# Kernel optimization log

Measured on AMD Instinct MI355X. Metric: run time of the kernel, lower is better.

The kernel has to match this reference:

```python
import jax, jax.numpy as jnp
import numpy as np

DIM = 128        # per-head dim == model width in this module
Q_HEADS = 16
KV_HEADS = 4
WINDOW = 512
BATCH = 4
SEQ = 2048


def setup_inputs() -> dict:
    key = jax.random.key(0)
    k1, k2, k3 = jax.random.split(key, 3)
    x = jax.random.normal(k1, (BATCH, SEQ, DIM), dtype=jnp.float32)
    # fused qkv weight, stored (in, out) so forward is x @ W_qkv
    W_qkv = jax.random.normal(k2, (DIM, (Q_HEADS + 2 * KV_HEADS) * DIM), dtype=jnp.float32) * (DIM ** -0.5)
    W_proj = jax.random.normal(k3, (Q_HEADS * DIM, DIM), dtype=jnp.float32) * ((Q_HEADS * DIM) ** -0.5)
    return {"x": x, "W_qkv": W_qkv, "W_proj": W_proj}


def _gqa_forward(x, W_qkv, W_proj):
    b, s, d = x.shape
    qkv = x @ W_qkv                                    # [b, s, (Hq+2Hkv)*d]
    qkv = qkv.reshape(b, s, Q_HEADS + 2 * KV_HEADS, d).transpose(0, 2, 1, 3)
    q = qkv[:, :Q_HEADS]                               # [b, Hq, s, d]
    k = qkv[:, Q_HEADS:Q_HEADS + KV_HEADS]             # [b, Hkv, s, d]
    v = qkv[:, Q_HEADS + KV_HEADS:]                    # [b, Hkv, s, d]

    # GQA: repeat kv heads to match q heads
    group = Q_HEADS // KV_HEADS
    k = jnp.repeat(k, group, axis=1)                   # [b, Hq, s, d]
    v = jnp.repeat(v, group, axis=1)

    scale = 1.0 / jnp.sqrt(jnp.float32(d))
    scores = jnp.einsum('bhqd,bhkd->bhqk', q, k) * scale   # [b, Hq, s, s]

    q_idx = jnp.arange(s)[:, None]
    kv_idx = jnp.arange(s)[None, :]
    rel = (q_idx - kv_idx).astype(jnp.float32)         # [s, s]
    # per-head ALiBi slope: exp2(-(h+1)*8/Hq), added (sign matches source)
    h = jnp.arange(Q_HEADS, dtype=jnp.float32)
    slopes = jnp.exp2(-((h + 1.0) * 8.0 / Q_HEADS))    # [Hq]
    scores = scores + slopes[None, :, None, None] * rel[None, None, :, :]

    mask = (q_idx >= kv_idx) & ((q_idx - kv_idx) <= WINDOW)
    scores = jnp.where(mask[None, None], scores, -jnp.inf)
    probs = jax.nn.softmax(scores, axis=-1)

    att = jnp.einsum('bhqk,bhkd->bhqd', probs, v)      # [b, Hq, s, d]
    att = att.transpose(0, 2, 1, 3).reshape(b, s, Q_HEADS * d)
    return att @ W_proj                                # [b, s, d]


def reference(x, W_qkv, W_proj):
    return _gqa_forward(x, W_qkv, W_proj)
```

## Files before the change

### kernel.cpp

```cpp
#include <hip/hip_runtime.h>
#include <math.h>

#define DIM_    128
#define QH_     16
#define KVH_    4
#define WIN_    512
#define BATCH_  4
#define SEQ_    2048
#define QKV_LD  3072
#define ATT_LD  2048

#define NX   (BATCH_*SEQ_*DIM_)
#define NWQ  (DIM_*QKV_LD)
#define NWP  (ATT_LD*DIM_)

typedef __attribute__((ext_vector_type(8))) short short8;
typedef __attribute__((ext_vector_type(4))) float f32x4;
typedef unsigned short u16;
typedef unsigned int u32;

__device__ __forceinline__ u16 f2bf(float f) {
    u32 u = __float_as_uint(f);
    u += 0x7fff + ((u >> 16) & 1);
    return (u16)(u >> 16);
}
__device__ __forceinline__ float bf2f(u16 u) {
    return __uint_as_float(((u32)u) << 16);
}
__device__ __forceinline__ u32 pkbf(float a, float b) {
    u32 r;
    __asm__("v_cvt_pk_bf16_f32 %0, %1, %2" : "=v"(r) : "v"(a), "v"(b));
    return r;
}
#define MFMA16 __builtin_amdgcn_mfma_f32_16x16x32_bf16

#if __has_builtin(__builtin_amdgcn_exp2f)
#define EXP2F __builtin_amdgcn_exp2f
#else
#define EXP2F exp2f
#endif

__device__ __forceinline__ void gload_lds16(const u16* g, u16* l) {
    __builtin_amdgcn_global_load_lds(
        (const __attribute__((address_space(1))) unsigned int*)(const void*)g,
        (__attribute__((address_space(3))) unsigned int*)(void*)l, 16, 0, 0);
}

__global__ __launch_bounds__(256) void prep(
    const float* __restrict__ x, const float* __restrict__ Wqkv,
    const float* __restrict__ Wproj,
    u16* __restrict__ xh, u16* __restrict__ wth, u16* __restrict__ wpth)
{
    if (blockIdx.x < 1024) {
        const size_t t = (size_t)blockIdx.x * 256 + threadIdx.x;
        float4 v = *(const float4*)(x + 4 * t);
        ushort4 o;
        o.x = f2bf(v.x); o.y = f2bf(v.y); o.z = f2bf(v.z); o.w = f2bf(v.w);
        *(ushort4*)(xh + 4 * t) = o;
        return;
    }
    __shared__ float T[32][33];
    int tile = blockIdx.x - 1024;
    const float* src; u16* dst; int K, N;
    if (tile < 384) { src = Wqkv;  dst = wth;  K = 128;  N = 3072; }
    else { tile -= 384; src = Wproj; dst = wpth; K = 2048; N = 128; }
    const int ntile = N >> 5;
    const int k0 = (tile / ntile) << 5, n0 = (tile % ntile) << 5;
    const int tx = threadIdx.x & 31, ty = threadIdx.x >> 5;
    #pragma unroll
    for (int i = 0; i < 4; ++i)
        T[ty + 8 * i][tx] = src[(size_t)(k0 + ty + 8 * i) * N + n0 + tx];
    __syncthreads();
    #pragma unroll
    for (int i = 0; i < 4; ++i)
        dst[(size_t)(n0 + ty + 8 * i) * K + k0 + tx] = f2bf(T[tx][ty + 8 * i]);
}

__global__ __launch_bounds__(256) void gemm1_mfma(
    const u16* __restrict__ xh, const u16* __restrict__ wth,
    u16* __restrict__ qkvb, u16* __restrict__ vg)
{
    const int bn = blockIdx.x * 64;
    const int mc = blockIdx.y * 512;
    const int wv = threadIdx.x >> 6, lane = threadIdx.x & 63;
    const int lo = lane & 15, hi = lane >> 4;
    const int lr = lo, quad = hi;

    short8 bf[4][4];
    #pragma unroll
    for (int nt = 0; nt < 4; ++nt)
        #pragma unroll
        for (int s = 0; s < 4; ++s)
            bf[nt][s] = *(const short8*)(
                wth + (size_t)(bn + nt * 16 + lo) * DIM_ + s * 32 + hi * 8);

    const bool qk = (bn < 2560);
    const u16* aA = xh + (size_t)(mc + wv * 16 + lo) * DIM_ + hi * 8;

#define G1BODY(AF, IT) do {                                                   \
    f32x4 acc[4] = {};                                                        \
    if (qk) {                                                                 \
        _Pragma("unroll")                                                     \
        for (int s = 0; s < 4; ++s)                                           \
            _Pragma("unroll")                                                 \
            for (int nt = 0; nt < 4; ++nt)                                    \
                acc[nt] = MFMA16(bf[nt][s], AF[s], acc[nt], 0, 0, 0);         \
        const int row = mc + (IT) * 64 + wv * 16 + lr;                        \
        u16* dst = qkvb + (size_t)row * QKV_LD + bn + quad * 4;               \
        _Pragma("unroll")                                                     \
        for (int nt = 0; nt < 4; ++nt) {                                      \
            uint2 o;                                                          \
            o.x = pkbf(acc[nt][0], acc[nt][1]);                               \
            o.y = pkbf(acc[nt][2], acc[nt][3]);                               \
            *(uint2*)(dst + nt * 16) = o;                                     \
        }                                                                     \
    } else {                                                                  \
        _Pragma("unroll")                                                     \
        for (int s = 0; s < 4; ++s)                                           \
            _Pragma("unroll")                                                 \
            for (int nt = 0; nt < 4; ++nt)                                    \
                acc[nt] = MFMA16(AF[s], bf[nt][s], acc[nt], 0, 0, 0);         \
        const int m0 = mc + (IT) * 64 + wv * 16 + quad * 4;                   \
        const int bb = m0 >> 11, mseq = m0 & 2047;                            \
        _Pragma("unroll")                                                     \
        for (int nt = 0; nt < 4; ++nt) {                                      \
            const int ncol = bn + nt * 16 + lr - 2560;                        \
            const int kvh = ncol >> 7, d = ncol & 127;                        \
            uint2 o;                                                          \
            o.x = pkbf(acc[nt][0], acc[nt][1]);                               \
            o.y = pkbf(acc[nt][2], acc[nt][3]);                               \
            *(uint2*)(vg + ((size_t)(bb * KVH_ + kvh) * DIM_ + d) * SEQ_      \
                      + mseq) = o;                                            \
        }                                                                     \
    }                                                                         \
} while (0)

    short8 afA[4], afB[4];
    #pragma unroll
    for (int s = 0; s < 4; ++s) afA[s] = *(const short8*)(aA + s * 32);

    #pragma unroll 1
    for (int it = 0; it < 8; it += 2) {
        const u16* aN = aA + (size_t)(it + 1) * 64 * DIM_;
        #pragma unroll
        for (int s = 0; s < 4; ++s) afB[s] = *(const short8*)(aN + s * 32);
        G1BODY(afA, it);
        const int nx = (it + 2 < 8) ? (it + 2) : 7;
        const u16* aN2 = aA + (size_t)nx * 64 * DIM_;
        #pragma unroll
        for (int s = 0; s < 4; ++s) afA[s] = *(const short8*)(aN2 + s * 32);
        G1BODY(afB, it + 1);
    }
#undef G1BODY
}

__global__ __launch_bounds__(512) void attn_mfma(
    const u16* __restrict__ qkvb, const u16* __restrict__ vg,
    u16* __restrict__ ah, int qoff)
{
    const int xcd  = blockIdx.x & 7;
    const int idx  = blockIdx.x >> 3;
    const int pair = xcd + 8 * (idx & 1);
    const int qt   = (idx >> 1) + qoff;
    const int b    = pair >> 2, kvh = pair & 3;
    const int q0 = qt << 5;
    const int tid = threadIdx.x;
    const int wv8 = tid >> 6, lane = tid & 63;
    const int hq = wv8 >> 1, mrow = wv8 & 1;
    const int lr = lane & 15, quad = lane >> 4;
    const int h = kvh * 4 + hq;
    const bool oddq = (quad & 1) != 0;

    __shared__ u16 Kb[3][8][512];
    __shared__ u16 Vb[3][8][512];

    const float scale2 = 0.08838834764831845f * 1.4426950408889634f;
    const float slope2 = exp2f(-0.5f * (float)(h + 1)) * 1.4426950408889634f;
    const int jbase = max(0, q0 - WIN_);
    const int nch = (q0 + 32 - jbase) >> 5;
    const size_t rowb = (size_t)b * SEQ_;
    const u16* kg  = qkvb + rowb * QKV_LD + (QH_ + kvh) * DIM_;
    const u16* vgb = vg + (size_t)(b * KVH_ + kvh) * DIM_ * SEQ_;
    const int lo = lane & 15, hi = lane >> 4;

    short8 qf[4];
    {
        const u16* qp = qkvb + (rowb + q0 + mrow * 16 + lr) * QKV_LD
                        + h * DIM_ + quad * 8;
        #pragma unroll
        for (int s = 0; s < 4; ++s) qf[s] = *(const short8*)(qp + 32 * s);
    }

    float alpha0;
    {
        const int q = q0 + mrow * 16 + lr;
        const int rm = (q < WIN_) ? q : WIN_;
        alpha0 = slope2 * (float)(q - rm);
    }

    f32x4 O[8] = {};
    float rs = 0.f;

    #define STAGE(CH, SLOT) do {                                              \
        const int _jk = jbase + ((CH) << 5);                                  \
        gload_lds16(kg + (size_t)(_jk + (wv8 >> 2) * 16 + lo) * QKV_LD        \
                    + (wv8 & 3) * 32 + hi * 8, &Kb[(SLOT)][wv8][0]);          \
        gload_lds16(vgb + (size_t)(wv8 * 16 + lo) * SEQ_ + _jk + hi * 8,      \
                    &Vb[(SLOT)][wv8][0]);                                     \
    } while (0)

    STAGE(0, 0);
    STAGE(1, 1);

    for (int ch = 0; ch < nch; ++ch) {
        const int jk = jbase + (ch << 5);
        const int slot = ch % 3;
        __asm__ volatile("s_waitcnt vmcnt(2)" ::: "memory");
        __asm__ volatile("s_barrier" ::: "memory");
        { const int cn = (ch + 2 < nch) ? (ch + 2) : (nch - 1);
          STAGE(cn, (ch + 2) % 3); }

        u32 pw[2][2];
        const int qm0 = q0 + mrow * 16;
        #pragma unroll
        for (int nt = 0; nt < 2; ++nt) {
            f32x4 c = {0.f, 0.f, 0.f, 0.f};
            __builtin_amdgcn_s_setprio(1);
            #pragma unroll
            for (int s = 0; s < 4; ++s) {
                short8 kf = *(const short8*)&Kb[slot][nt * 4 + s][lane * 8];
                c = MFMA16(kf, qf[s], c, 0, 0, 0);
            }
            __builtin_amdgcn_s_setprio(0);
            const int jknt = jk + nt * 16;
            const float b0 = fmaf(-slope2, (float)(jknt + quad * 4), alpha0);
            float e0, e1, e2, e3;
            if (qm0 >= jknt + 15 && qm0 + 15 <= jknt + WIN_) {
                e0 = EXP2F(fmaf(c[0], scale2, b0));
                e1 = EXP2F(fmaf(c[1], scale2, b0 - slope2));
                e2 = EXP2F(fmaf(c[2], scale2, b0 - 2.f * slope2));
                e3 = EXP2F(fmaf(c[3], scale2, b0 - 3.f * slope2));
            } else {
                const int q = qm0 + lr, j0q = jknt + quad * 4;
                float ee[4];
                #pragma unroll
                for (int r = 0; r < 4; ++r) {
                    const int rel = q - (j0q + r);
                    const float t = fmaf(c[r], scale2, b0 - (float)r * slope2);
                    ee[r] = ((unsigned)rel <= (unsigned)WIN_) ? EXP2F(t) : 0.f;
                }
                e0 = ee[0]; e1 = ee[1]; e2 = ee[2]; e3 = ee[3];
            }
            rs += (e0 + e1) + (e2 + e3);
            pw[nt][0] = pkbf(e0, e1);
            pw[nt][1] = pkbf(e2, e3);
        }

        short8 pa;
        {
            union { u32 w[4]; short8 s; } P;
            #pragma unroll
            for (int w = 0; w < 2; ++w) {
                auto r = __builtin_amdgcn_permlane32_swap(
                    pw[0][w], pw[1][w], false, false);
                const u32 rx = r[0], ry = r[1];
                const u32 sx = (u32)__shfl_xor((int)rx, 16);
                const u32 sy = (u32)__shfl_xor((int)ry, 16);
                P.w[w]     = oddq ? sy : rx;
                P.w[2 + w] = oddq ? ry : sx;
            }
            pa = P.s;
        }

        __builtin_amdgcn_s_setprio(1);
        #pragma unroll
        for (int nt = 0; nt < 8; ++nt) {
            short8 vf = *(const short8*)&Vb[slot][nt][lane * 8];
            O[nt] = MFMA16(vf, pa, O[nt], 0, 0, 0);
        }
        __builtin_amdgcn_s_setprio(0);
    }
    #undef STAGE

    __asm__ volatile("s_waitcnt vmcnt(0)" ::: "memory");

    rs += __shfl_xor(rs, 16);
    rs += __shfl_xor(rs, 32);

    {
        const float inv = 1.0f / rs;
        u16* dst = ah + (rowb + q0 + mrow * 16 + lr) * (size_t)ATT_LD
                   + h * DIM_;
        #pragma unroll
        for (int nt = 0; nt < 8; ++nt) {
            uint2 o;
            o.x = pkbf(O[nt][0] * inv, O[nt][1] * inv);
            o.y = pkbf(O[nt][2] * inv, O[nt][3] * inv);
            *(uint2*)(dst + nt * 16 + quad * 4) = o;
        }
    }
}

__global__ __launch_bounds__(256) void gemm2_mfma(
    const u16* __restrict__ ah, const u16* __restrict__ wpth,
    float* __restrict__ out)
{
    const int bm = blockIdx.x * 16;
    const int wv = threadIdx.x >> 6, lane = threadIdx.x & 63;
    const int lr = lane & 15, quad = lane >> 4;
    const int cq = wv;

    const u16* arow  = ah + (size_t)(bm + lr) * ATT_LD + quad * 8;
    const u16* w0row = wpth + (size_t)(cq * 32 + lr) * ATT_LD + quad * 8;
    const u16* w1row = w0row + (size_t)16 * ATT_LD;

    f32x4 acc0 = {0.f, 0.f, 0.f, 0.f}, acc1 = {0.f, 0.f, 0.f, 0.f};
    #pragma unroll 8
    for (int k0 = 0; k0 < ATT_LD; k0 += 32) {
        short8 a  = *(const short8*)(arow + k0);
        short8 w0 = *(const short8*)(w0row + k0);
        short8 w1 = *(const short8*)(w1row + k0);
        acc0 = MFMA16(w0, a, acc0, 0, 0, 0);
        acc1 = MFMA16(w1, a, acc1, 0, 0, 0);
    }
    float* orow = out + (size_t)(bm + lr) * DIM_ + cq * 32;
    *(float4*)(orow + quad * 4)      = *(float4*)&acc0;
    *(float4*)(orow + 16 + quad * 4) = *(float4*)&acc1;
}

extern "C" void kernel_launch(void* const* d_in, const int* in_sizes, int n_in,
                              void* d_out, int out_size, void* d_ws, size_t ws_size,
                              hipStream_t stream)
{
    const float* x     = (const float*)d_in[0];
    const float* Wqkv  = (const float*)d_in[1];
    const float* Wproj = (const float*)d_in[2];
    float* out = (float*)d_out;

    u16* xh   = (u16*)d_ws;
    u16* wth  = xh   + (size_t)NX;
    u16* wpth = wth  + (size_t)NWQ;
    u16* qkvb = wpth + (size_t)NWP;
    u16* vg   = qkvb + (size_t)8192 * QKV_LD;
    u16* ahp  = vg   + (size_t)BATCH_ * KVH_ * DIM_ * SEQ_;

    prep<<<1024 + 640, 256, 0, stream>>>(x, Wqkv, Wproj, xh, wth, wpth);

    gemm1_mfma<<<dim3(48, 16), 256, 0, stream>>>(xh, wth, qkvb, vg);

    attn_mfma<<<512, 512, 0, stream>>>(qkvb, vg, ahp, 0);
    attn_mfma<<<512, 512, 0, stream>>>(qkvb, vg, ahp, 32);

    gemm2_mfma<<<8192 / 16, 256, 0, stream>>>(ahp, wpth, out);
}
```

Baseline: 202.2 us.

## Tile output projection GEMM through LDS with triple-buffered async loads

Reworks the output-projection GEMM so each block handles 64 rows with 8 waves in a 2x4 wave grid. A and W chunks are staged into shared memory with direct global-to-LDS loads in a three-slot ring, using waitcnt and a barrier per chunk. The goal is to reuse W across more rows and overlap loads with MFMA, where previously every wave streamed its operands straight from global memory. In exchange it launches only 128 blocks, which may underfill the GPU, and adds barrier and LDS overhead.

```diff
diff --git a/kernel.cpp b/kernel.cpp
--- a/kernel.cpp
+++ b/kernel.cpp
@@ -301,31 +301,76 @@
     }
 }
 
-__global__ __launch_bounds__(256) void gemm2_mfma(
+__global__ __launch_bounds__(512) void gemm2_mfma(
     const u16* __restrict__ ah, const u16* __restrict__ wpth,
     float* __restrict__ out)
 {
-    const int bm = blockIdx.x * 16;
-    const int wv = threadIdx.x >> 6, lane = threadIdx.x & 63;
+    const int bm = blockIdx.x * 64;
+    const int tid = threadIdx.x;
+    const int wv8 = tid >> 6, lane = tid & 63;
+    const int wr = wv8 >> 2, wc = wv8 & 3;
     const int lr = lane & 15, quad = lane >> 4;
-    const int cq = wv;
-
-    const u16* arow  = ah + (size_t)(bm + lr) * ATT_LD + quad * 8;
-    const u16* w0row = wpth + (size_t)(cq * 32 + lr) * ATT_LD + quad * 8;
-    const u16* w1row = w0row + (size_t)16 * ATT_LD;
-
-    f32x4 acc0 = {0.f, 0.f, 0.f, 0.f}, acc1 = {0.f, 0.f, 0.f, 0.f};
-    #pragma unroll 8
-    for (int k0 = 0; k0 < ATT_LD; k0 += 32) {
-        short8 a  = *(const short8*)(arow + k0);
-        short8 w0 = *(const short8*)(w0row + k0);
-        short8 w1 = *(const short8*)(w1row + k0);
-        acc0 = MFMA16(w0, a, acc0, 0, 0, 0);
-        acc1 = MFMA16(w1, a, acc1, 0, 0, 0);
-    }
-    float* orow = out + (size_t)(bm + lr) * DIM_ + cq * 32;
-    *(float4*)(orow + quad * 4)      = *(float4*)&acc0;
-    *(float4*)(orow + 16 + quad * 4) = *(float4*)&acc1;
+    const int lo = lr, hi = quad;
+
+    __shared__ u16 At[3][8][512];
+    __shared__ u16 Wt[3][16][512];
+
+    #define G2STAGE(CH, SLOT) do {                                            \
+        const int _jk = (CH) << 6;                                            \
+        {   const int _mt = wv8 >> 1, _s = wv8 & 1;        \
+            gload_lds16(ah + (size_t)(bm + _mt * 16 + lo) * ATT_LD            \
+                        + _jk + _s * 32 + hi * 8, &At[(SLOT)][wv8][0]); }     \
+        _Pragma("unroll")                                                     \
+        for (int _t = 0; _t < 2; ++_t) {               \
+            const int _p = wv8 + _t * 8;                                      \
+            const int _nt = _p >> 1, _s = _p & 1;                             \
+            gload_lds16(wpth + (size_t)(_nt * 16 + lo) * ATT_LD               \
+                        + _jk + _s * 32 + hi * 8, &Wt[(SLOT)][_p][0]);        \
+        }                                                                     \
+    } while (0)
+
+    f32x4 acc[2][2] = {};
+
+    G2STAGE(0, 0);
+    G2STAGE(1, 1);
+
+    for (int ch = 0; ch < 32; ++ch) {
+        const int slot = ch % 3;
+        __asm__ volatile("s_waitcnt vmcnt(3)" ::: "memory");
+        __asm__ volatile("s_barrier" ::: "memory");
+        { const int cn = (ch + 2 < 32) ? (ch + 2) : 31;
+          G2STAGE(cn, (ch + 2) % 3); }
+
+        #pragma unroll
+        for (int s = 0; s < 2; ++s) {
+            short8 af[2], wf[2];
+            #pragma unroll
+            for (int mt = 0; mt < 2; ++mt)
+                af[mt] = *(const short8*)&At[slot][(wr * 2 + mt) * 2 + s][lane * 8];
+            #pragma unroll
+            for (int nt = 0; nt < 2; ++nt)
+                wf[nt] = *(const short8*)&Wt[slot][(wc * 2 + nt) * 2 + s][lane * 8];
+            __builtin_amdgcn_s_setprio(1);
+            #pragma unroll
+            for (int mt = 0; mt < 2; ++mt)
+                #pragma unroll
+                for (int nt = 0; nt < 2; ++nt)
+                    acc[mt][nt] = MFMA16(wf[nt], af[mt], acc[mt][nt], 0, 0, 0);
+            __builtin_amdgcn_s_setprio(0);
+        }
+    }
+    #undef G2STAGE
+
+    __asm__ volatile("s_waitcnt vmcnt(0)" ::: "memory");
+
+    #pragma unroll
+    for (int mt = 0; mt < 2; ++mt)
+        #pragma unroll
+        for (int nt = 0; nt < 2; ++nt) {
+            float* orow = out + (size_t)(bm + (wr * 2 + mt) * 16 + lr) * DIM_
+                          + (wc * 2 + nt) * 16 + quad * 4;
+            *(float4*)orow = *(float4*)&acc[mt][nt];
+        }
 }
 
 extern "C" void kernel_launch(void* const* d_in, const int* in_sizes, int n_in,
@@ -351,5 +396,5 @@
     attn_mfma<<<512, 512, 0, stream>>>(qkvb, vg, ahp, 0);
     attn_mfma<<<512, 512, 0, stream>>>(qkvb, vg, ahp, 32);
 
-    gemm2_mfma<<<8192 / 16, 256, 0, stream>>>(ahp, wpth, out);
-}
+    gemm2_mfma<<<8192 / 64, 512, 0, stream>>>(ahp, wpth, out);
+}
```

Result: no change. 198.4 us (-1.9%).
